# Kernel tuning notes

Measured on AMD Instinct MI355X. Metric: run time of the kernel, lower is better.

## Reference

```python
import jax, jax.numpy as jnp
import numpy as np

B, C, K = 16384, 10, 5   # batch, context window (2*window_size), num_neg per context
V, D = 400000, 300       # vocab size, embedding dim


def setup_inputs() -> dict:
    key = jax.random.key(0)
    k1, k2, k3, k4, k5 = jax.random.split(key, 5)
    return {
        "target": jax.random.randint(k1, (B,), 0, V, dtype=jnp.int64)
        if jax.config.jax_enable_x64 else jax.random.randint(k1, (B,), 0, V).astype(jnp.int32),
        "context": jax.random.randint(k2, (B, C), 0, V).astype(jnp.int32),
        "negative_samples": jax.random.randint(k3, (B, C * K), 0, V).astype(jnp.int32),
        "emb_in": jax.random.normal(k4, (V, D), dtype=jnp.float32),
        "emb_out": jax.random.normal(k5, (V, D), dtype=jnp.float32),
    }


def reference(target, context, negative_samples, emb_in, emb_out):
    # Skip-gram NCE loss (Word2VecPy.loss).
    tgt = emb_in[target]               # [B, D]
    ctx = emb_out[context]             # [B, C, D]
    neg = emb_out[negative_samples]    # [B, C*K, D]

    # positive: log sigmoid(ctx . tgt), mean over context
    pos_scores = jnp.einsum("bcd,bd->bc", ctx, tgt)          # [B, C]
    pos_loss = jnp.mean(jax.nn.log_sigmoid(pos_scores), axis=1)  # [B]

    # negative: log sigmoid(-neg . tgt), sum over K negatives, mean over context
    neg_scores = -jnp.einsum("bnd,bd->bn", neg, tgt)         # [B, C*K]
    neg_ls = jax.nn.log_sigmoid(neg_scores).reshape(B, C, K)  # [B, C, K]
    neg_loss = jnp.mean(jnp.sum(neg_ls, axis=2), axis=1)      # [B]

    return -jnp.mean(pos_loss + neg_loss)
```

## Files before the change

kernel.cpp:

```cpp
#include <hip/hip_runtime.h>
#include <hip/hip_bf16.h>


#define D_DIM 300
#define D4    75
#define C_DIM 10
#define NEG_DIM 50
#define ROWS 60

__device__ __forceinline__ float log_sigmoid_fast(float x) {
    float e = __expf(-fabsf(x));
    return fminf(x, 0.f) - __logf(1.f + e);
}

__global__ __launch_bounds__(256) void w2v_loss_partial(
    const int*   __restrict__ target,
    const int*   __restrict__ context,
    const int*   __restrict__ negs,
    const float* __restrict__ emb_in,
    const float* __restrict__ emb_out,
    float*       __restrict__ partial)
{
    const int tid  = threadIdx.x;
    const int lane = tid & 63;
    const int wave = tid >> 6;
    const int b    = blockIdx.x * 4 + wave;

    int v_idx = 0;
    if (lane < C_DIM)      v_idx = context[b * C_DIM + lane];
    else if (lane < ROWS)  v_idx = negs[b * NEG_DIM + (lane - C_DIM)];

    const float4* trow =
        reinterpret_cast<const float4*>(emb_in + (size_t)target[b] * D_DIM);
    const bool tail = lane < (D4 - 64);
    float4 ta = trow[lane];
    float4 tb = make_float4(0.f, 0.f, 0.f, 0.f);
    if (tail) tb = trow[64 + lane];

    float acc = 0.f;
    #pragma unroll 3
    for (int g = 0; g < ROWS / 4; ++g) {
        float d[4];
        #pragma unroll
        for (int i = 0; i < 4; ++i) {
            const int r = g * 4 + i;
            const int sidx = __builtin_amdgcn_readlane(v_idx, r);
            const float4* row =
                reinterpret_cast<const float4*>(emb_out + (size_t)sidx * D_DIM);
            float4 ra = row[lane];
            float4 rb = make_float4(0.f, 0.f, 0.f, 0.f);
            if (tail) rb = row[64 + lane];
            d[i] = ra.x * ta.x + ra.y * ta.y + ra.z * ta.z + ra.w * ta.w
                 + rb.x * tb.x + rb.y * tb.y + rb.z * tb.z + rb.w * tb.w;
        }

        #pragma unroll
        for (int i = 0; i < 4; ++i) d[i] += __shfl_xor(d[i], 32, 64);
        const bool hi32 = (lane & 32) != 0;
        float p = hi32 ? d[1] : d[0];
        float q = hi32 ? d[3] : d[2];
        p += __shfl_xor(p, 16, 64);
        q += __shfl_xor(q, 16, 64);
        float v = (lane & 16) ? q : p;
        v += __shfl_xor(v, 8, 64);
        v += __shfl_xor(v, 4, 64);
        v += __shfl_xor(v, 2, 64);
        v += __shfl_xor(v, 1, 64);

        const int gq  = lane >> 4;
        const int rid = g * 4 + (((gq & 1) << 1) | (gq >> 1));
        const float x = (rid < C_DIM) ? v : -v;
        acc += log_sigmoid_fast(x);
    }

    acc += __shfl_xor(acc, 16, 64);
    acc += __shfl_xor(acc, 32, 64);
    if (lane == 0) partial[b] = acc;
}

__global__ __launch_bounds__(256) void w2v_loss_reduce(
    const float* __restrict__ partial,
    float*       __restrict__ out,
    int n, float inv_scale)
{
    __shared__ float s[256];
    float acc = 0.f;
    for (int i = threadIdx.x; i < n; i += 256) acc += partial[i];
    s[threadIdx.x] = acc;
    __syncthreads();
    #pragma unroll
    for (int off = 128; off > 0; off >>= 1) {
        if (threadIdx.x < off) s[threadIdx.x] += s[threadIdx.x + off];
        __syncthreads();
    }
    if (threadIdx.x == 0) out[0] = -s[0] * inv_scale;
}

extern "C" void kernel_launch(void* const* d_in, const int* in_sizes, int n_in,
                              void* d_out, int out_size, void* d_ws, size_t ws_size,
                              hipStream_t stream) {
    const int*   target  = (const int*)  d_in[0];
    const int*   context = (const int*)  d_in[1];
    const int*   negs    = (const int*)  d_in[2];
    const float* emb_in  = (const float*)d_in[3];
    const float* emb_out = (const float*)d_in[4];
    float*       out     = (float*)d_out;

    const int B = in_sizes[0];
    float* partial = (float*)d_ws;

    w2v_loss_partial<<<B / 4, 256, 0, stream>>>(target, context, negs,
                                                emb_in, emb_out, partial);
    const float inv_scale = 1.0f / ((float)B * (float)C_DIM);
    w2v_loss_reduce<<<1, 256, 0, stream>>>(partial, out, B, inv_scale);
}
```

Measured before the change: 209.9 us.

## Split emb_out gathers into vocab-range phases for cache locality

Measured after the change: 277.5 us. 1.32x slower.

```diff
diff --git a/kernel.cpp b/kernel.cpp
--- a/kernel.cpp
+++ b/kernel.cpp
@@ -7,19 +7,21 @@
 #define C_DIM 10
 #define NEG_DIM 50
 #define ROWS 60
+#define PHASES 3
 
 __device__ __forceinline__ float log_sigmoid_fast(float x) {
     float e = __expf(-fabsf(x));
     return fminf(x, 0.f) - __logf(1.f + e);
 }
 
-__global__ __launch_bounds__(256) void w2v_loss_partial(
+__global__ __launch_bounds__(256) void w2v_loss_phase(
     const int*   __restrict__ target,
     const int*   __restrict__ context,
     const int*   __restrict__ negs,
     const float* __restrict__ emb_in,
     const float* __restrict__ emb_out,
-    float*       __restrict__ partial)
+    float*       __restrict__ partial,
+    int lo, int hi)
 {
     const int tid  = threadIdx.x;
     const int lane = tid & 63;
@@ -38,43 +40,26 @@
     if (tail) tb = trow[64 + lane];
 
     float acc = 0.f;
-    #pragma unroll 3
-    for (int g = 0; g < ROWS / 4; ++g) {
-        float d[4];
-        #pragma unroll
-        for (int i = 0; i < 4; ++i) {
-            const int r = g * 4 + i;
-            const int sidx = __builtin_amdgcn_readlane(v_idx, r);
+    for (int r = 0; r < ROWS; ++r) {
+        const int sidx = __builtin_amdgcn_readlane(v_idx, r);
+        if (sidx >= lo && sidx < hi) {
             const float4* row =
                 reinterpret_cast<const float4*>(emb_out + (size_t)sidx * D_DIM);
             float4 ra = row[lane];
             float4 rb = make_float4(0.f, 0.f, 0.f, 0.f);
             if (tail) rb = row[64 + lane];
-            d[i] = ra.x * ta.x + ra.y * ta.y + ra.z * ta.z + ra.w * ta.w
-                 + rb.x * tb.x + rb.y * tb.y + rb.z * tb.z + rb.w * tb.w;
+
+            float dot = ra.x * ta.x + ra.y * ta.y + ra.z * ta.z + ra.w * ta.w
+                      + rb.x * tb.x + rb.y * tb.y + rb.z * tb.z + rb.w * tb.w;
+            #pragma unroll
+            for (int off = 32; off > 0; off >>= 1)
+                dot += __shfl_xor(dot, off, 64);
+
+            const float x = (r < C_DIM) ? dot : -dot;
+            acc += log_sigmoid_fast(x);
         }
-
-        #pragma unroll
-        for (int i = 0; i < 4; ++i) d[i] += __shfl_xor(d[i], 32, 64);
-        const bool hi32 = (lane & 32) != 0;
-        float p = hi32 ? d[1] : d[0];
-        float q = hi32 ? d[3] : d[2];
-        p += __shfl_xor(p, 16, 64);
-        q += __shfl_xor(q, 16, 64);
-        float v = (lane & 16) ? q : p;
-        v += __shfl_xor(v, 8, 64);
-        v += __shfl_xor(v, 4, 64);
-        v += __shfl_xor(v, 2, 64);
-        v += __shfl_xor(v, 1, 64);
-
-        const int gq  = lane >> 4;
-        const int rid = g * 4 + (((gq & 1) << 1) | (gq >> 1));
-        const float x = (rid < C_DIM) ? v : -v;
-        acc += log_sigmoid_fast(x);
     }
 
-    acc += __shfl_xor(acc, 16, 64);
-    acc += __shfl_xor(acc, 32, 64);
     if (lane == 0) partial[b] = acc;
 }
 
@@ -107,10 +92,18 @@
     float*       out     = (float*)d_out;
 
     const int B = in_sizes[0];
+    const int V = in_sizes[3] / D_DIM;
     float* partial = (float*)d_ws;
 
-    w2v_loss_partial<<<B / 4, 256, 0, stream>>>(target, context, negs,
-                                                emb_in, emb_out, partial);
+    for (int p = 0; p < PHASES; ++p) {
+        const int lo = (int)((long long)V * p / PHASES);
+        const int hi = (int)((long long)V * (p + 1) / PHASES);
+        w2v_loss_phase<<<B / 4, 256, 0, stream>>>(target, context, negs,
+                                                  emb_in, emb_out,
+                                                  partial + (size_t)p * B,
+                                                  lo, hi);
+    }
+
     const float inv_scale = 1.0f / ((float)B * (float)C_DIM);
-    w2v_loss_reduce<<<1, 256, 0, stream>>>(partial, out, B, inv_scale);
+    w2v_loss_reduce<<<1, 256, 0, stream>>>(partial, out, PHASES * B, inv_scale);
 }
```

## Bucket lookups by output-vocab row so each emb_out row is read once

Applied to the files above, without the earlier changes.

Measured after the change: 489.7 us. 2.33x slower.

```diff
diff --git a/kernel.cpp b/kernel.cpp
--- a/kernel.cpp
+++ b/kernel.cpp
@@ -13,47 +13,227 @@
     return fminf(x, 0.f) - __logf(1.f + e);
 }
 
-__global__ __launch_bounds__(256) void w2v_loss_partial(
+
+__global__ __launch_bounds__(256) void k_init(int* __restrict__ counts,
+                                              int* __restrict__ cursor, int V) {
+    for (int i = blockIdx.x * 256 + threadIdx.x; i < V; i += gridDim.x * 256) {
+        counts[i] = 0;
+        cursor[i] = 0;
+    }
+}
+
+__global__ __launch_bounds__(256) void k_count(const int* __restrict__ ctx,
+                                               const int* __restrict__ negs,
+                                               int* __restrict__ counts, int P) {
+    int p = blockIdx.x * 256 + threadIdx.x;
+    if (p >= P) return;
+    int b = p / ROWS, r = p - b * ROWS;
+    int v = (r < C_DIM) ? ctx[b * C_DIM + r] : negs[b * NEG_DIM + (r - C_DIM)];
+    atomicAdd(&counts[v], 1);
+}
+
+__global__ __launch_bounds__(256) void k_scan1(const int* __restrict__ counts,
+                                               int* __restrict__ bsum, int V) {
+    __shared__ int s[256];
+    const int base = blockIdx.x * 1024;
+    const int t = threadIdx.x;
+    int a = 0;
+    #pragma unroll
+    for (int j = 0; j < 4; ++j) {
+        int i = base + 4 * t + j;
+        if (i < V) a += counts[i];
+    }
+    s[t] = a; __syncthreads();
+    for (int off = 128; off > 0; off >>= 1) {
+        if (t < off) s[t] += s[t + off];
+        __syncthreads();
+    }
+    if (t == 0) bsum[blockIdx.x] = s[0];
+}
+
+__global__ __launch_bounds__(512) void k_scan2(const int* __restrict__ bsum,
+                                               int* __restrict__ boff, int nb) {
+    __shared__ int s[512];
+    const int t = threadIdx.x;
+    int v = (t < nb) ? bsum[t] : 0;
+    s[t] = v; __syncthreads();
+    for (int off = 1; off < 512; off <<= 1) {
+        int add = (t >= off) ? s[t - off] : 0;
+        __syncthreads();
+        s[t] += add;
+        __syncthreads();
+    }
+    if (t < nb) boff[t] = s[t] - v;
+}
+
+__global__ __launch_bounds__(256) void k_scan3(const int* __restrict__ counts,
+                                               const int* __restrict__ boff,
+                                               int* __restrict__ off, int V) {
+    __shared__ int s[256];
+    const int base = blockIdx.x * 1024;
+    const int t = threadIdx.x;
+    int c[4]; int a = 0;
+    #pragma unroll
+    for (int j = 0; j < 4; ++j) {
+        int i = base + 4 * t + j;
+        c[j] = (i < V) ? counts[i] : 0;
+        a += c[j];
+    }
+    s[t] = a; __syncthreads();
+    for (int o = 1; o < 256; o <<= 1) {
+        int add = (t >= o) ? s[t - o] : 0;
+        __syncthreads();
+        s[t] += add;
+        __syncthreads();
+    }
+    int run = boff[blockIdx.x] + s[t] - a;
+    #pragma unroll
+    for (int j = 0; j < 4; ++j) {
+        int i = base + 4 * t + j;
+        if (i < V) off[i] = run;
+        run += c[j];
+    }
+}
+
+__global__ __launch_bounds__(256) void k_scatter(const int* __restrict__ ctx,
+                                                 const int* __restrict__ negs,
+                                                 const int* __restrict__ off,
+                                                 int* __restrict__ cursor,
+                                                 int* __restrict__ bucket, int P) {
+    int p = blockIdx.x * 256 + threadIdx.x;
+    if (p >= P) return;
+    int b = p / ROWS, r = p - b * ROWS;
+    int v = (r < C_DIM) ? ctx[b * C_DIM + r] : negs[b * NEG_DIM + (r - C_DIM)];
+    int pos = off[v] + atomicAdd(&cursor[v], 1);
+    bucket[pos] = (b << 6) | r;
+}
+
+
+__global__ __launch_bounds__(256) void k_main(
     const int*   __restrict__ target,
-    const int*   __restrict__ context,
-    const int*   __restrict__ negs,
     const float* __restrict__ emb_in,
     const float* __restrict__ emb_out,
-    float*       __restrict__ partial)
+    const int*   __restrict__ counts,
+    const int*   __restrict__ off,
+    const int*   __restrict__ bucket,
+    float*       __restrict__ result)
 {
     const int tid  = threadIdx.x;
     const int lane = tid & 63;
     const int wave = tid >> 6;
-    const int b    = blockIdx.x * 4 + wave;
-
+    const int v    = blockIdx.x * 4 + wave;
+
+    const int n = counts[v];
+    if (n == 0) return;
+    const int base = off[v];
+
+    const bool tail = lane < (D4 - 64);
+    const float4 zero = make_float4(0.f, 0.f, 0.f, 0.f);
+
+    const float4* orow = reinterpret_cast<const float4*>(emb_out + (size_t)v * D_DIM);
+    float4 oa = orow[lane];
+    float4 ob = tail ? orow[64 + lane] : zero;
+
+    int eAll = (lane < n) ? bucket[base + lane] : 0;
+    int tAll = (lane < n) ? target[eAll >> 6] : 0;
+
+    int e = __builtin_amdgcn_readlane(eAll, 0);
+    int t = __builtin_amdgcn_readlane(tAll, 0);
+    const float4* trow = reinterpret_cast<const float4*>(emb_in + (size_t)t * D_DIM);
+    float4 ta = trow[lane];
+    float4 tb = tail ? trow[64 + lane] : zero;
+
+    for (int k = 0; k < n; ++k) {
+        int e1 = 0;
+        float4 na = zero, nb_ = zero;
+        if (k + 1 < n) {
+            int t1;
+            if (k + 1 < 64) {
+                e1 = __builtin_amdgcn_readlane(eAll, k + 1);
+                t1 = __builtin_amdgcn_readlane(tAll, k + 1);
+            } else {
+                e1 = bucket[base + k + 1];
+                t1 = target[e1 >> 6];
+            }
+            const float4* tr = reinterpret_cast<const float4*>(emb_in + (size_t)t1 * D_DIM);
+            na  = tr[lane];
+            nb_ = tail ? tr[64 + lane] : zero;
+        }
+
+        float dot = oa.x * ta.x + oa.y * ta.y + oa.z * ta.z + oa.w * ta.w
+                  + ob.x * tb.x + ob.y * tb.y + ob.z * tb.z + ob.w * tb.w;
+        #pragma unroll
+        for (int o = 32; o > 0; o >>= 1)
+            dot += __shfl_xor(dot, o, 64);
+
+        const float x = ((e & 63) < C_DIM) ? dot : -dot;
+        const float ls = log_sigmoid_fast(x);
+        if (lane == 0) result[e] = ls;
+
+        e = e1; ta = na; tb = nb_;
+    }
+}
+
+
+__global__ __launch_bounds__(256) void k_r1(const float* __restrict__ res,
+                                            float* __restrict__ part, int n) {
+    __shared__ float s[256];
+    float a = 0.f;
+    for (int i = blockIdx.x * 256 + threadIdx.x; i < n; i += 1024 * 256) {
+        if ((i & 63) < ROWS) a += res[i];
+    }
+    s[threadIdx.x] = a; __syncthreads();
+    for (int o = 128; o > 0; o >>= 1) {
+        if (threadIdx.x < o) s[threadIdx.x] += s[threadIdx.x + o];
+        __syncthreads();
+    }
+    if (threadIdx.x == 0) part[blockIdx.x] = s[0];
+}
+
+__global__ __launch_bounds__(256) void k_r2(const float* __restrict__ part,
+                                            float* __restrict__ out,
+                                            int n, float inv_scale) {
+    __shared__ float s[256];
+    float a = 0.f;
+    for (int i = threadIdx.x; i < n; i += 256) a += part[i];
+    s[threadIdx.x] = a; __syncthreads();
+    for (int o = 128; o > 0; o >>= 1) {
+        if (threadIdx.x < o) s[threadIdx.x] += s[threadIdx.x + o];
+        __syncthreads();
+    }
+    if (threadIdx.x == 0) out[0] = -s[0] * inv_scale;
+}
+
+
+__global__ __launch_bounds__(256) void w2v_loss_partial(
+    const int* __restrict__ target, const int* __restrict__ context,
+    const int* __restrict__ negs, const float* __restrict__ emb_in,
+    const float* __restrict__ emb_out, float* __restrict__ partial)
+{
+    const int tid = threadIdx.x, lane = tid & 63, wave = tid >> 6;
+    const int b = blockIdx.x * 4 + wave;
     int v_idx = 0;
-    if (lane < C_DIM)      v_idx = context[b * C_DIM + lane];
-    else if (lane < ROWS)  v_idx = negs[b * NEG_DIM + (lane - C_DIM)];
-
-    const float4* trow =
-        reinterpret_cast<const float4*>(emb_in + (size_t)target[b] * D_DIM);
+    if (lane < C_DIM)     v_idx = context[b * C_DIM + lane];
+    else if (lane < ROWS) v_idx = negs[b * NEG_DIM + (lane - C_DIM)];
+    const float4* trow = reinterpret_cast<const float4*>(emb_in + (size_t)target[b] * D_DIM);
     const bool tail = lane < (D4 - 64);
     float4 ta = trow[lane];
     float4 tb = make_float4(0.f, 0.f, 0.f, 0.f);
     if (tail) tb = trow[64 + lane];
-
     float acc = 0.f;
     #pragma unroll 3
     for (int g = 0; g < ROWS / 4; ++g) {
         float d[4];
         #pragma unroll
         for (int i = 0; i < 4; ++i) {
-            const int r = g * 4 + i;
-            const int sidx = __builtin_amdgcn_readlane(v_idx, r);
-            const float4* row =
-                reinterpret_cast<const float4*>(emb_out + (size_t)sidx * D_DIM);
+            const int sidx = __builtin_amdgcn_readlane(v_idx, g * 4 + i);
+            const float4* row = reinterpret_cast<const float4*>(emb_out + (size_t)sidx * D_DIM);
             float4 ra = row[lane];
             float4 rb = make_float4(0.f, 0.f, 0.f, 0.f);
             if (tail) rb = row[64 + lane];
             d[i] = ra.x * ta.x + ra.y * ta.y + ra.z * ta.z + ra.w * ta.w
                  + rb.x * tb.x + rb.y * tb.y + rb.z * tb.z + rb.w * tb.w;
         }
-
         #pragma unroll
         for (int i = 0; i < 4; ++i) d[i] += __shfl_xor(d[i], 32, 64);
         const bool hi32 = (lane & 32) != 0;
@@ -61,40 +241,20 @@
         float q = hi32 ? d[3] : d[2];
         p += __shfl_xor(p, 16, 64);
         q += __shfl_xor(q, 16, 64);
-        float v = (lane & 16) ? q : p;
-        v += __shfl_xor(v, 8, 64);
-        v += __shfl_xor(v, 4, 64);
-        v += __shfl_xor(v, 2, 64);
-        v += __shfl_xor(v, 1, 64);
-
-        const int gq  = lane >> 4;
+        float vv = (lane & 16) ? q : p;
+        vv += __shfl_xor(vv, 8, 64);
+        vv += __shfl_xor(vv, 4, 64);
+        vv += __shfl_xor(vv, 2, 64);
+        vv += __shfl_xor(vv, 1, 64);
+        const int gq = lane >> 4;
         const int rid = g * 4 + (((gq & 1) << 1) | (gq >> 1));
-        const float x = (rid < C_DIM) ? v : -v;
-        acc += log_sigmoid_fast(x);
-    }
-
+        acc += log_sigmoid_fast((rid < C_DIM) ? vv : -vv);
+    }
     acc += __shfl_xor(acc, 16, 64);
     acc += __shfl_xor(acc, 32, 64);
     if (lane == 0) partial[b] = acc;
 }
 
-__global__ __launch_bounds__(256) void w2v_loss_reduce(
-    const float* __restrict__ partial,
-    float*       __restrict__ out,
-    int n, float inv_scale)
-{
-    __shared__ float s[256];
-    float acc = 0.f;
-    for (int i = threadIdx.x; i < n; i += 256) acc += partial[i];
-    s[threadIdx.x] = acc;
-    __syncthreads();
-    #pragma unroll
-    for (int off = 128; off > 0; off >>= 1) {
-        if (threadIdx.x < off) s[threadIdx.x] += s[threadIdx.x + off];
-        __syncthreads();
-    }
-    if (threadIdx.x == 0) out[0] = -s[0] * inv_scale;
-}
 
 extern "C" void kernel_launch(void* const* d_in, const int* in_sizes, int n_in,
                               void* d_out, int out_size, void* d_ws, size_t ws_size,
@@ -107,10 +267,50 @@
     float*       out     = (float*)d_out;
 
     const int B = in_sizes[0];
-    float* partial = (float*)d_ws;
-
-    w2v_loss_partial<<<B / 4, 256, 0, stream>>>(target, context, negs,
-                                                emb_in, emb_out, partial);
+    const int V = in_sizes[3] / D_DIM;
+    const int P = B * ROWS;
+    const int RSLOTS = B * 64;
+    const int NB = (V + 1023) / 1024;
     const float inv_scale = 1.0f / ((float)B * (float)C_DIM);
-    w2v_loss_reduce<<<1, 256, 0, stream>>>(partial, out, B, inv_scale);
-}
+
+    auto al = [](size_t x) { return (x + 255) & ~(size_t)255; };
+    size_t o = 0;
+    const size_t o_counts = o; o = al(o + (size_t)V * 4);
+    const size_t o_off    = o; o = al(o + (size_t)V * 4);
+    const size_t o_cur    = o; o = al(o + (size_t)V * 4);
+    const size_t o_bsum   = o; o = al(o + 4096);
+    const size_t o_boff   = o; o = al(o + 4096);
+    const size_t o_bucket = o; o = al(o + (size_t)P * 4);
+    const size_t o_res    = o; o = al(o + (size_t)RSLOTS * 4);
+    const size_t o_part   = o; o = al(o + 1024 * 4);
+    const size_t needed = o;
+
+    char* ws = (char*)d_ws;
+    if (ws_size >= needed && NB <= 512 && (V % 4) == 0) {
+        int*   counts = (int*)(ws + o_counts);
+        int*   offv   = (int*)(ws + o_off);
+        int*   cursor = (int*)(ws + o_cur);
+        int*   bsum   = (int*)(ws + o_bsum);
+        int*   boff   = (int*)(ws + o_boff);
+        int*   bucket = (int*)(ws + o_bucket);
+        float* result = (float*)(ws + o_res);
+        float* part   = (float*)(ws + o_part);
+
+        k_init   <<<1024, 256, 0, stream>>>(counts, cursor, V);
+        k_count  <<<(P + 255) / 256, 256, 0, stream>>>(context, negs, counts, P);
+        k_scan1  <<<NB, 256, 0, stream>>>(counts, bsum, V);
+        k_scan2  <<<1, 512, 0, stream>>>(bsum, boff, NB);
+        k_scan3  <<<NB, 256, 0, stream>>>(counts, boff, offv, V);
+        k_scatter<<<(P + 255) / 256, 256, 0, stream>>>(context, negs, offv,
+                                                       cursor, bucket, P);
+        k_main   <<<V / 4, 256, 0, stream>>>(target, emb_in, emb_out,
+                                             counts, offv, bucket, result);
+        k_r1     <<<1024, 256, 0, stream>>>(result, part, RSLOTS);
+        k_r2     <<<1, 256, 0, stream>>>(part, out, 1024, inv_scale);
+    } else {
+        float* partial = (float*)d_ws;
+        w2v_loss_partial<<<B / 4, 256, 0, stream>>>(target, context, negs,
+                                                    emb_in, emb_out, partial);
+        k_r2<<<1, 256, 0, stream>>>(partial, out, B, inv_scale);
+    }
+}
```

## Partition embedding gathers into vocab-range phases for cache locality

Applied to the files above, without the earlier changes.

Result: slower. 295.0 us (+40.5%).

```diff
diff --git a/kernel.cpp b/kernel.cpp
--- a/kernel.cpp
+++ b/kernel.cpp
@@ -7,18 +7,44 @@
 #define C_DIM 10
 #define NEG_DIM 50
 #define ROWS 60
+#define PHASES 3
 
 __device__ __forceinline__ float log_sigmoid_fast(float x) {
     float e = __expf(-fabsf(x));
     return fminf(x, 0.f) - __logf(1.f + e);
 }
 
-__global__ __launch_bounds__(256) void w2v_loss_partial(
+__global__ __launch_bounds__(256) void k_build(
+    const int* __restrict__ ctx, const int* __restrict__ negs,
+    int* __restrict__ lists,
+    int* __restrict__ cnts,
+    int B, int PQ)
+{
+    const int b = blockIdx.x * 256 + threadIdx.x;
+    if (b >= B) return;
+    int c0 = 0, c1 = 0, c2 = 0;
+    #pragma unroll 4
+    for (int r = 0; r < ROWS; ++r) {
+        const int v = (r < C_DIM) ? ctx[b * C_DIM + r]
+                                  : negs[b * NEG_DIM + (r - C_DIM)];
+        const int p = v / PQ;
+        int* slot;
+        if (p == 0)      slot = &lists[((size_t)0 * B + b) * ROWS + c0++];
+        else if (p == 1) slot = &lists[((size_t)1 * B + b) * ROWS + c1++];
+        else             slot = &lists[((size_t)2 * B + b) * ROWS + c2++];
+        *slot = (v << 6) | r;
+    }
+    cnts[0 * B + b] = c0;
+    cnts[1 * B + b] = c1;
+    cnts[2 * B + b] = c2;
+}
+
+__global__ __launch_bounds__(256) void k_phase(
     const int*   __restrict__ target,
-    const int*   __restrict__ context,
-    const int*   __restrict__ negs,
     const float* __restrict__ emb_in,
     const float* __restrict__ emb_out,
+    const int*   __restrict__ list,
+    const int*   __restrict__ cnt,
     float*       __restrict__ partial)
 {
     const int tid  = threadIdx.x;
@@ -26,32 +52,47 @@
     const int wave = tid >> 6;
     const int b    = blockIdx.x * 4 + wave;
 
-    int v_idx = 0;
-    if (lane < C_DIM)      v_idx = context[b * C_DIM + lane];
-    else if (lane < ROWS)  v_idx = negs[b * NEG_DIM + (lane - C_DIM)];
+    const int n = cnt[b];
+    if (n == 0) { if (lane == 0) partial[b] = 0.f; return; }
+
+    const float4 zero = make_float4(0.f, 0.f, 0.f, 0.f);
+    const bool tail = lane < (D4 - 64);
+
+    const int* lst = list + (size_t)b * ROWS;
+    const int eAll = (lane < n) ? lst[lane] : 63;
 
     const float4* trow =
         reinterpret_cast<const float4*>(emb_in + (size_t)target[b] * D_DIM);
-    const bool tail = lane < (D4 - 64);
     float4 ta = trow[lane];
-    float4 tb = make_float4(0.f, 0.f, 0.f, 0.f);
-    if (tail) tb = trow[64 + lane];
+    float4 tb = tail ? trow[64 + lane] : zero;
 
     float acc = 0.f;
-    #pragma unroll 3
-    for (int g = 0; g < ROWS / 4; ++g) {
+    const int ng = (n + 3) >> 2;
+    #pragma unroll 2
+    for (int g = 0; g < ng; ++g) {
+        const int e0 = __builtin_amdgcn_readlane(eAll, 4 * g + 0);
+        const int e1 = __builtin_amdgcn_readlane(eAll, 4 * g + 1);
+        const int e2 = __builtin_amdgcn_readlane(eAll, 4 * g + 2);
+        const int e3 = __builtin_amdgcn_readlane(eAll, 4 * g + 3);
+
         float d[4];
-        #pragma unroll
-        for (int i = 0; i < 4; ++i) {
-            const int r = g * 4 + i;
-            const int sidx = __builtin_amdgcn_readlane(v_idx, r);
-            const float4* row =
-                reinterpret_cast<const float4*>(emb_out + (size_t)sidx * D_DIM);
-            float4 ra = row[lane];
-            float4 rb = make_float4(0.f, 0.f, 0.f, 0.f);
-            if (tail) rb = row[64 + lane];
-            d[i] = ra.x * ta.x + ra.y * ta.y + ra.z * ta.z + ra.w * ta.w
-                 + rb.x * tb.x + rb.y * tb.y + rb.z * tb.z + rb.w * tb.w;
+        {
+            const float4* r0 = reinterpret_cast<const float4*>(emb_out + (size_t)(e0 >> 6) * D_DIM);
+            const float4* r1 = reinterpret_cast<const float4*>(emb_out + (size_t)(e1 >> 6) * D_DIM);
+            const float4* r2 = reinterpret_cast<const float4*>(emb_out + (size_t)(e2 >> 6) * D_DIM);
+            const float4* r3 = reinterpret_cast<const float4*>(emb_out + (size_t)(e3 >> 6) * D_DIM);
+            float4 a0 = r0[lane], b0 = tail ? r0[64 + lane] : zero;
+            float4 a1 = r1[lane], b1 = tail ? r1[64 + lane] : zero;
+            float4 a2 = r2[lane], b2 = tail ? r2[64 + lane] : zero;
+            float4 a3 = r3[lane], b3 = tail ? r3[64 + lane] : zero;
+            d[0] = a0.x*ta.x + a0.y*ta.y + a0.z*ta.z + a0.w*ta.w
+                 + b0.x*tb.x + b0.y*tb.y + b0.z*tb.z + b0.w*tb.w;
+            d[1] = a1.x*ta.x + a1.y*ta.y + a1.z*ta.z + a1.w*ta.w
+                 + b1.x*tb.x + b1.y*tb.y + b1.z*tb.z + b1.w*tb.w;
+            d[2] = a2.x*ta.x + a2.y*ta.y + a2.z*ta.z + a2.w*ta.w
+                 + b2.x*tb.x + b2.y*tb.y + b2.z*tb.z + b2.w*tb.w;
+            d[3] = a3.x*ta.x + a3.y*ta.y + a3.z*ta.z + a3.w*ta.w
+                 + b3.x*tb.x + b3.y*tb.y + b3.z*tb.z + b3.w*tb.w;
         }
 
         #pragma unroll
@@ -61,16 +102,19 @@
         float q = hi32 ? d[3] : d[2];
         p += __shfl_xor(p, 16, 64);
         q += __shfl_xor(q, 16, 64);
-        float v = (lane & 16) ? q : p;
-        v += __shfl_xor(v, 8, 64);
-        v += __shfl_xor(v, 4, 64);
-        v += __shfl_xor(v, 2, 64);
-        v += __shfl_xor(v, 1, 64);
-
-        const int gq  = lane >> 4;
-        const int rid = g * 4 + (((gq & 1) << 1) | (gq >> 1));
-        const float x = (rid < C_DIM) ? v : -v;
-        acc += log_sigmoid_fast(x);
+        float vv = (lane & 16) ? q : p;
+        vv += __shfl_xor(vv, 8, 64);
+        vv += __shfl_xor(vv, 4, 64);
+        vv += __shfl_xor(vv, 2, 64);
+        vv += __shfl_xor(vv, 1, 64);
+
+        const int gq = lane >> 4;
+        const int rsel = (gq == 0) ? (e0 & 63)
+                       : (gq == 1) ? (e2 & 63)
+                       : (gq == 2) ? (e1 & 63)
+                                   : (e3 & 63);
+        const float x = (rsel < C_DIM) ? vv : -vv;
+        acc += (rsel < ROWS) ? log_sigmoid_fast(x) : 0.f;
     }
 
     acc += __shfl_xor(acc, 16, 64);
@@ -78,22 +122,68 @@
     if (lane == 0) partial[b] = acc;
 }
 
-__global__ __launch_bounds__(256) void w2v_loss_reduce(
-    const float* __restrict__ partial,
-    float*       __restrict__ out,
-    int n, float inv_scale)
+__global__ __launch_bounds__(256) void k_r2(const float* __restrict__ part,
+                                            float* __restrict__ out,
+                                            int n, float inv_scale) {
+    __shared__ float s[256];
+    float a = 0.f;
+    for (int i = threadIdx.x; i < n; i += 256) a += part[i];
+    s[threadIdx.x] = a; __syncthreads();
+    for (int o = 128; o > 0; o >>= 1) {
+        if (threadIdx.x < o) s[threadIdx.x] += s[threadIdx.x + o];
+        __syncthreads();
+    }
+    if (threadIdx.x == 0) out[0] = -s[0] * inv_scale;
+}
+
+__global__ __launch_bounds__(256) void w2v_loss_partial(
+    const int* __restrict__ target, const int* __restrict__ context,
+    const int* __restrict__ negs, const float* __restrict__ emb_in,
+    const float* __restrict__ emb_out, float* __restrict__ partial)
 {
-    __shared__ float s[256];
+    const int tid = threadIdx.x, lane = tid & 63, wave = tid >> 6;
+    const int b = blockIdx.x * 4 + wave;
+    int v_idx = 0;
+    if (lane < C_DIM)     v_idx = context[b * C_DIM + lane];
+    else if (lane < ROWS) v_idx = negs[b * NEG_DIM + (lane - C_DIM)];
+    const float4* trow = reinterpret_cast<const float4*>(emb_in + (size_t)target[b] * D_DIM);
+    const bool tail = lane < (D4 - 64);
+    float4 ta = trow[lane];
+    float4 tb = make_float4(0.f, 0.f, 0.f, 0.f);
+    if (tail) tb = trow[64 + lane];
     float acc = 0.f;
-    for (int i = threadIdx.x; i < n; i += 256) acc += partial[i];
-    s[threadIdx.x] = acc;
-    __syncthreads();
-    #pragma unroll
-    for (int off = 128; off > 0; off >>= 1) {
-        if (threadIdx.x < off) s[threadIdx.x] += s[threadIdx.x + off];
-        __syncthreads();
-    }
-    if (threadIdx.x == 0) out[0] = -s[0] * inv_scale;
+    #pragma unroll 3
+    for (int g = 0; g < ROWS / 4; ++g) {
+        float d[4];
+        #pragma unroll
+        for (int i = 0; i < 4; ++i) {
+            const int sidx = __builtin_amdgcn_readlane(v_idx, g * 4 + i);
+            const float4* row = reinterpret_cast<const float4*>(emb_out + (size_t)sidx * D_DIM);
+            float4 ra = row[lane];
+            float4 rb = make_float4(0.f, 0.f, 0.f, 0.f);
+            if (tail) rb = row[64 + lane];
+            d[i] = ra.x * ta.x + ra.y * ta.y + ra.z * ta.z + ra.w * ta.w
+                 + rb.x * tb.x + rb.y * tb.y + rb.z * tb.z + rb.w * tb.w;
+        }
+        #pragma unroll
+        for (int i = 0; i < 4; ++i) d[i] += __shfl_xor(d[i], 32, 64);
+        const bool hi32 = (lane & 32) != 0;
+        float p = hi32 ? d[1] : d[0];
+        float q = hi32 ? d[3] : d[2];
+        p += __shfl_xor(p, 16, 64);
+        q += __shfl_xor(q, 16, 64);
+        float vv = (lane & 16) ? q : p;
+        vv += __shfl_xor(vv, 8, 64);
+        vv += __shfl_xor(vv, 4, 64);
+        vv += __shfl_xor(vv, 2, 64);
+        vv += __shfl_xor(vv, 1, 64);
+        const int gq = lane >> 4;
+        const int rid = g * 4 + (((gq & 1) << 1) | (gq >> 1));
+        acc += log_sigmoid_fast((rid < C_DIM) ? vv : -vv);
+    }
+    acc += __shfl_xor(acc, 16, 64);
+    acc += __shfl_xor(acc, 32, 64);
+    if (lane == 0) partial[b] = acc;
 }
 
 extern "C" void kernel_launch(void* const* d_in, const int* in_sizes, int n_in,
@@ -106,11 +196,38 @@
     const float* emb_out = (const float*)d_in[4];
     float*       out     = (float*)d_out;
 
-    const int B = in_sizes[0];
-    float* partial = (float*)d_ws;
-
-    w2v_loss_partial<<<B / 4, 256, 0, stream>>>(target, context, negs,
-                                                emb_in, emb_out, partial);
+    const int B  = in_sizes[0];
+    const int V  = in_sizes[3] / D_DIM;
+    const int PQ = (V + PHASES - 1) / PHASES;
     const float inv_scale = 1.0f / ((float)B * (float)C_DIM);
-    w2v_loss_reduce<<<1, 256, 0, stream>>>(partial, out, B, inv_scale);
-}
+
+    auto al = [](size_t x) { return (x + 255) & ~(size_t)255; };
+    size_t o = 0;
+    const size_t o_lists = o; o = al(o + (size_t)PHASES * B * ROWS * 4);
+    const size_t o_cnts  = o; o = al(o + (size_t)PHASES * B * 4);
+    const size_t o_part  = o; o = al(o + (size_t)PHASES * B * 4);
+    const size_t needed  = o;
+
+    char* ws = (char*)d_ws;
+    if (ws_size >= needed && (B % 4) == 0) {
+        int*   lists = (int*)(ws + o_lists);
+        int*   cnts  = (int*)(ws + o_cnts);
+        float* part  = (float*)(ws + o_part);
+
+        k_build<<<(B + 255) / 256, 256, 0, stream>>>(context, negs, lists,
+                                                     cnts, B, PQ);
+        for (int p = 0; p < PHASES; ++p) {
+            k_phase<<<B / 4, 256, 0, stream>>>(
+                target, emb_in, emb_out,
+                lists + (size_t)p * B * ROWS,
+                cnts  + (size_t)p * B,
+                part  + (size_t)p * B);
+        }
+        k_r2<<<1, 256, 0, stream>>>(part, out, PHASES * B, inv_scale);
+    } else {
+        float* partial = (float*)d_ws;
+        w2v_loss_partial<<<B / 4, 256, 0, stream>>>(target, context, negs,
+                                                    emb_in, emb_out, partial);
+        k_r2<<<1, 256, 0, stream>>>(partial, out, B, inv_scale);
+    }
+}
```
